# Kernel optimization log

Hardware: AMD Instinct MI355X
Metric: run time of the kernel (lower is better)

Reference implementation:

```python
import jax, jax.numpy as jnp
import numpy as np


def lrelu(x):
    return jax.nn.leaky_relu(x, 0.1)


def mask_softmax(a, mask, axis=-1):
    # faithful to the torch version: max over ALL entries, mask applied post-exp
    a_max = jnp.max(a, axis=axis, keepdims=True)
    e = jnp.exp(a - a_max) * mask
    return e / (jnp.sum(e, axis=axis, keepdims=True) + 1e-6)


def gru_cell(x, h, w_ih, w_hh, b_ih, b_hh):
    # torch.nn.GRUCell math; weights stored as [in, 3H]
    gi = x @ w_ih + b_ih
    gh = h @ w_hh + b_hh
    ir, iz, inn = jnp.split(gi, 3, axis=-1)
    hr, hz, hn = jnp.split(gh, 3, axis=-1)
    r = jax.nn.sigmoid(ir + hr)
    z = jax.nn.sigmoid(iz + hz)
    n = jnp.tanh(inn + r * hn)
    return (1 - z) * n + z * h


def setup_inputs() -> dict:
    key = jax.random.key(0)
    B, N, M, E, H, D, K = 128, 256, 12, 256, 128, 3, 2
    AF, BF, NA, NB = 82, 6, 100, 12
    ks = iter(jax.random.split(key, 64))
    nrm = lambda shape: jax.random.normal(next(ks), shape, jnp.float32) * 0.05
    return dict(
        batch_size=B,
        vertex_mask=jnp.ones((B, N), jnp.float32),
        vertex=jax.random.randint(next(ks), (B, N), 0, NA, dtype=jnp.int32),
        edge=jax.random.randint(next(ks), (B, E), 0, NB, dtype=jnp.int32),
        atom_adj=jax.random.randint(next(ks), (B * N * M,), 0, B * N, dtype=jnp.int32),
        bond_adj=jax.random.randint(next(ks), (B * N * M,), 0, B * E, dtype=jnp.int32),
        nbs_mask=jnp.ones((B, N, M), jnp.float32),
        init_atom_features=nrm((NA, AF)),
        init_bond_features=nrm((NB, BF)),
        emb_w=nrm((AF, H)), emb_b=nrm((H,)),
        Wa_main_w=nrm((D, K, H, H)), Wa_main_b=nrm((D, K, H)),
        Wbmm_w=nrm((D, K, H)), Wbmm_b=nrm((D, K)),
        Wmain_w=nrm((D, K, H, H)), Wmain_b=nrm((D, K, H)),
        Wm2s_w=nrm((D, K * H, H)), Wm2s_b=nrm((D, H)),
        Ws2m_w=nrm((D, H, H)), Ws2m_b=nrm((D, H)),
        Wsuper_w=nrm((D, H, H)), Wsuper_b=nrm((D, H)),
        Wzm1_w=nrm((D, H, H)), Wzm1_b=nrm((D, H)),
        Wzm2_w=nrm((D, H, H)), Wzm2_b=nrm((D, H)),
        Wzs1_w=nrm((D, H, H)), Wzs1_b=nrm((D, H)),
        Wzs2_w=nrm((D, H, H)), Wzs2_b=nrm((D, H)),
        U2_w=nrm((D, H + BF, H)), U2_b=nrm((D, H)),
        U1_w=nrm((D, 2 * H, H)), U1_b=nrm((D, H)),
        gm_wih=nrm((H, 3 * H)), gm_whh=nrm((H, 3 * H)), gm_bih=nrm((3 * H,)), gm_bhh=nrm((3 * H,)),
        gs_wih=nrm((H, 3 * H)), gs_whh=nrm((H, 3 * H)), gs_bih=nrm((3 * H,)), gs_bhh=nrm((3 * H,)),
    )


def reference(batch_size, vertex_mask, vertex, edge, atom_adj, bond_adj, nbs_mask,
              init_atom_features, init_bond_features, emb_w, emb_b,
              Wa_main_w, Wa_main_b, Wbmm_w, Wbmm_b, Wmain_w, Wmain_b,
              Wm2s_w, Wm2s_b, Ws2m_w, Ws2m_b, Wsuper_w, Wsuper_b,
              Wzm1_w, Wzm1_b, Wzm2_w, Wzm2_b, Wzs1_w, Wzs1_b, Wzs2_w, Wzs2_b,
              U2_w, U2_b, U1_w, U1_b,
              gm_wih, gm_whh, gm_bih, gm_bhh, gs_wih, gs_whh, gs_bih, gs_bhh):
    B = batch_size
    N = vertex_mask.shape[1]
    M = nbs_mask.shape[2]
    H = emb_w.shape[1]
    BF = init_bond_features.shape[1]
    D, K = Wa_main_w.shape[0], Wa_main_w.shape[1]

    vertex_initial = init_atom_features[vertex]          # [B,N,AF]
    edge_initial = init_bond_features[edge]              # [B,E,BF]
    vf = lrelu(vertex_initial @ emb_w + emb_b)           # [B,N,H]
    vm = vertex_mask[:, :, None]
    sf = jnp.sum(vf * vm, axis=1, keepdims=True)         # [B,1,H] super node

    for d in range(D):
        # multi-head super-node attention (all k heads vectorized)
        a_main = jnp.tanh(jnp.einsum('bnh,khg->bkng', vf, Wa_main_w[d]) + Wa_main_b[d][None, :, None, :])
        a = jnp.einsum('bkng,kg->bkn', a_main * sf[:, None, :, :], Wbmm_w[d]) + Wbmm_b[d][None, :, None]
        attn = mask_softmax(a, vertex_mask[:, None, :])                  # [B,K,N]
        wv = jnp.einsum('bnh,khg->bkng', vf, Wmain_w[d]) + Wmain_b[d][None, :, None, :]
        m = jnp.einsum('bkn,bkng->bkg', attn, wv).reshape(B, 1, K * H)   # head-concat
        main_to_super = jnp.tanh(m @ Wm2s_w[d] + Wm2s_b[d])              # [B,1,H]

        # WLN unit: gather neighbor atom/bond features, fused MLP + masked sum
        vnei = vf.reshape(-1, H)[atom_adj].reshape(B, N, M, H)
        enei = edge_initial.reshape(-1, BF)[bond_adj].reshape(B, N, M, BF)
        nei = jnp.concatenate([vnei, enei], axis=-1)                     # [B,N,M,H+BF]
        nei_label = lrelu(nei @ U2_w[d] + U2_b[d])
        nei_label = jnp.sum(nei_label * nbs_mask[..., None], axis=-2)    # [B,N,H]
        main_self = lrelu(jnp.concatenate([vf, nei_label], axis=-1) @ U1_w[d] + U1_b[d])

        super_to_main = jnp.tanh(sf @ Ws2m_w[d] + Ws2m_b[d])
        super_self = jnp.tanh(sf @ Wsuper_w[d] + Wsuper_b[d])

        z_main = jax.nn.sigmoid(main_self @ Wzm1_w[d] + Wzm1_b[d]
                                + super_to_main @ Wzm2_w[d] + Wzm2_b[d])
        hidden_main = (1 - z_main) * main_self + z_main * super_to_main
        vf = gru_cell(hidden_main.reshape(-1, H), vf.reshape(-1, H),
                      gm_wih, gm_whh, gm_bih, gm_bhh).reshape(B, N, H)

        z_super = jax.nn.sigmoid(super_self @ Wzs1_w[d] + Wzs1_b[d]
                                 + main_to_super @ Wzs2_w[d] + Wzs2_b[d])
        hidden_super = (1 - z_super) * super_self + z_super * main_to_super
        sf = gru_cell(hidden_super.reshape(B, H), sf.reshape(B, H),
                      gs_wih, gs_whh, gs_bih, gs_bhh).reshape(B, 1, H)

    return (vf, sf)
```

## Files before the change

### kernel.cpp

```cpp
#include <hip/hip_runtime.h>

typedef unsigned short ushort_t;
typedef unsigned int uint_t;
typedef __attribute__((ext_vector_type(8))) short short8;
typedef __attribute__((ext_vector_type(4))) float f32x4;

#define B   128
#define Nv  256
#define Mn  12
#define Hd  128
#define Dd  3
#define Kk  2
#define AFd 82
#define BFd 6
#define BN  (B*Nv)

enum { EPI_NONE = 0, EPI_LRELU = 1 };

__device__ __forceinline__ float lrelu(float x) { return fmaxf(x, 0.1f * x); }
__device__ __forceinline__ float sigmoidf(float x) { return 1.f / (1.f + expf(-x)); }
__device__ __forceinline__ ushort_t f2b(float x) {
    uint_t u = __float_as_uint(x);
    return (ushort_t)((u + 0x7FFFu + ((u >> 16) & 1u)) >> 16);
}
__device__ __forceinline__ float b2f(ushort_t s) {
    return __uint_as_float(((uint_t)s) << 16);
}
__device__ __forceinline__ void b2f4(uint2 u, float* o) {
    o[0] = __uint_as_float((u.x & 0xFFFFu) << 16);
    o[1] = __uint_as_float(u.x & 0xFFFF0000u);
    o[2] = __uint_as_float((u.y & 0xFFFFu) << 16);
    o[3] = __uint_as_float(u.y & 0xFFFF0000u);
}
__device__ __forceinline__ uint_t pk2(float lo, float hi) {
    return (uint_t)f2b(lo) | ((uint_t)f2b(hi) << 16);
}
__device__ __forceinline__ float upk_lo(uint_t u) { return __uint_as_float((u & 0xFFFFu) << 16); }
__device__ __forceinline__ float upk_hi(uint_t u) { return __uint_as_float(u & 0xFFFF0000u); }

struct PrepJob {
    const float* W;
    long sliceStride;
    int K, ldw, nPerSlice, Kspan, KpadRow, kDst, total, outOff, blockStart;
};
struct PrepJobs { PrepJob j[18]; int nJobs; };

__global__ __launch_bounds__(256) void k_prep_all(PrepJobs P, ushort_t* __restrict__ WT)
{
    int bid = blockIdx.x;
    int ji = 0;
    #pragma unroll 1
    while (ji + 1 < P.nJobs && P.j[ji + 1].blockStart <= bid) ++ji;
    const PrepJob J = P.j[ji];
    const int idx = (bid - J.blockStart) * 256 + threadIdx.x;
    if (idx >= J.total) return;
    const int n = idx / J.Kspan, k = idx % J.Kspan;
    const int slice = n / J.nPerSlice, nn = n % J.nPerSlice;
    float v = (k < J.K) ? J.W[(size_t)slice * J.sliceStride + (size_t)k * J.ldw + nn] : 0.f;
    WT[(size_t)J.outOff + (size_t)n * J.KpadRow + J.kDst + k] = f2b(v);
}

__global__ __launch_bounds__(256) void k_qtab(const float* __restrict__ init_bond,
                                              const float* __restrict__ U2w,
                                              ushort_t* __restrict__ qt)
{
    const int d = blockIdx.x;
    const float* W = U2w + (size_t)d * (Hd + BFd) * Hd + (size_t)Hd * Hd;
    ushort_t* q = qt + (size_t)d * 12 * Hd;
    for (int idx = threadIdx.x; idx < 12 * Hd; idx += 256) {
        const int j = idx >> 7, h = idx & 127;
        float s = 0.f;
        #pragma unroll
        for (int f = 0; f < BFd; ++f) s += init_bond[j * BFd + f] * W[f * Hd + h];
        q[idx] = f2b(s);
    }
}

template<int EPI, bool ABF, bool OBF>
__global__ __launch_bounds__(256) void mgemm(
    const void* __restrict__ A1v, int lda1, int K1,
    const int* __restrict__ rowidx,
    const ushort_t* __restrict__ Wt, int Kpad,
    const float* __restrict__ b1,
    void* __restrict__ outv, long ldo)
{
    const int t    = threadIdx.x;
    const int lane = t & 63;
    const int w    = t >> 6;
    const int wm   = w >> 1, wn = w & 1;
    const int lr   = lane & 15, lg = lane >> 4;
    const int row0 = blockIdx.x * 64;

    __shared__ ushort_t As[64 * 64];

    f32x4 acc[2][4];
    #pragma unroll
    for (int i = 0; i < 2; ++i)
        #pragma unroll
        for (int j = 0; j < 4; ++j)
            acc[i][j] = (f32x4){0.f, 0.f, 0.f, 0.f};

    const int r_st = t >> 2, q4 = t & 3;
    const int grow = row0 + r_st;
    const long arow = rowidx ? (long)rowidx[grow] : (long)grow;

    const int nck = Kpad >> 6;
    for (int ck = 0; ck < nck; ++ck) {
        if (ck) __syncthreads();
        {
            const int kb = ck * 64 + q4 * 16;
            union { ushort_t us[16]; uint4 qv[2]; } tmp;
            #pragma unroll
            for (int j = 0; j < 16; ++j) {
                const int kg = kb + j;
                ushort_t v = 0;
                if (kg < K1) {
                    if (ABF) v = ((const ushort_t*)A1v)[(size_t)arow * lda1 + kg];
                    else     v = f2b(((const float*)A1v)[(size_t)arow * lda1 + kg]);
                }
                tmp.us[j] = v;
            }
            #pragma unroll
            for (int j = 0; j < 2; ++j) {
                int byte = r_st * 128 + q4 * 32 + j * 16;
                byte ^= ((r_st & 7) << 4);
                *(uint4*)((char*)As + byte) = tmp.qv[j];
            }
        }
        __syncthreads();
        #pragma unroll
        for (int ks = 0; ks < 64; ks += 32) {
            short8 af[2], bfr[4];
            #pragma unroll
            for (int mf = 0; mf < 2; ++mf) {
                const int row = wm * 32 + mf * 16 + lr;
                int byte = row * 128 + (ks + lg * 8) * 2;
                byte ^= ((row & 7) << 4);
                af[mf] = *(const short8*)((const char*)As + byte);
            }
            #pragma unroll
            for (int nf = 0; nf < 4; ++nf) {
                const int col = wn * 64 + nf * 16 + lr;
                bfr[nf] = *(const short8*)(Wt + (size_t)col * Kpad + ck * 64 + ks + lg * 8);
            }
            #pragma unroll
            for (int mf = 0; mf < 2; ++mf)
                #pragma unroll
                for (int nf = 0; nf < 4; ++nf)
                    acc[mf][nf] = __builtin_amdgcn_mfma_f32_16x16x32_bf16(
                        af[mf], bfr[nf], acc[mf][nf], 0, 0, 0);
        }
    }

    #pragma unroll
    for (int mf = 0; mf < 2; ++mf) {
        #pragma unroll
        for (int nf = 0; nf < 4; ++nf) {
            const int c = wn * 64 + nf * 16 + lr;
            #pragma unroll
            for (int reg = 0; reg < 4; ++reg) {
                const int r = wm * 32 + mf * 16 + lg * 4 + reg;
                const size_t row = (size_t)row0 + r;
                float v = acc[mf][nf][reg];
                if (b1) v += b1[c];
                if constexpr (EPI == EPI_LRELU) v = lrelu(v);
                const size_t oidx = row * ldo + c;
                if (OBF) ((ushort_t*)outv)[oidx] = f2b(v);
                else     ((float*)outv)[oidx] = v;
            }
        }
    }
}

__global__ __launch_bounds__(256) void k_tdp(
    const ushort_t* __restrict__ vfb,
    const ushort_t* __restrict__ Wt,
    const float* __restrict__ waB,
    const float* __restrict__ u2B,
    const float* __restrict__ sf,
    const float* __restrict__ wbmmW,
    const float* __restrict__ wbmmB,
    float* __restrict__ a_out,
    ushort_t* __restrict__ Pout)
{
    const int t = threadIdx.x;
    const int lane = t & 63, w = t >> 6;
    const int wm = w >> 1, wn = w & 1;
    const int lr = lane & 15, lg = lane >> 4;
    const int row0 = blockIdx.x * 64;
    const int ky = blockIdx.y;
    const int b = row0 >> 8;

    __shared__ ushort_t As[64 * 128];
    __shared__ float EUs[128], EBb[128];
    __shared__ float red[64][2];

    {
        const int r_st = t >> 2, q4 = t & 3;
        const ushort_t* src = vfb + (size_t)(row0 + r_st) * Hd + q4 * 32;
        #pragma unroll
        for (int j = 0; j < 4; ++j) {
            uint4 v = ((const uint4*)src)[j];
            int byte = r_st * 256 + q4 * 64 + j * 16;
            byte ^= ((r_st & 7) << 4);
            *(uint4*)((char*)As + byte) = v;
        }
    }
    if (ky != 2 && t < 128) {
        EUs[t] = sf[b * Hd + t] * wbmmW[ky * Hd + t];
        EBb[t] = waB[ky * Hd + t];
    }
    __syncthreads();

    const ushort_t* Wty = Wt + (size_t)ky * 16384;

    f32x4 acc[2][4];
    #pragma unroll
    for (int i = 0; i < 2; ++i)
        #pragma unroll
        for (int j = 0; j < 4; ++j)
            acc[i][j] = (f32x4){0.f, 0.f, 0.f, 0.f};

    #pragma unroll
    for (int kk = 0; kk < 128; kk += 32) {
        short8 af[2], bfr[4];
        #pragma unroll
        for (int nf = 0; nf < 4; ++nf) {
            const int col = wn * 64 + nf * 16 + lr;
            bfr[nf] = *(const short8*)(Wty + (size_t)col * 128 + kk + lg * 8);
        }
        #pragma unroll
        for (int mf = 0; mf < 2; ++mf) {
            const int row = wm * 32 + mf * 16 + lr;
            int byte = row * 256 + (kk + lg * 8) * 2;
            byte ^= ((row & 7) << 4);
            af[mf] = *(const short8*)((const char*)As + byte);
        }
        #pragma unroll
        for (int mf = 0; mf < 2; ++mf)
            #pragma unroll
            for (int nf = 0; nf < 4; ++nf)
                acc[mf][nf] = __builtin_amdgcn_mfma_f32_16x16x32_bf16(
                    af[mf], bfr[nf], acc[mf][nf], 0, 0, 0);
    }

    if (ky == 2) {
        #pragma unroll
        for (int mf = 0; mf < 2; ++mf)
            #pragma unroll
            for (int nf = 0; nf < 4; ++nf) {
                const int c = wn * 64 + nf * 16 + lr;
                #pragma unroll
                for (int reg = 0; reg < 4; ++reg) {
                    const int r = wm * 32 + mf * 16 + lg * 4 + reg;
                    Pout[(size_t)(row0 + r) * Hd + c] = f2b(acc[mf][nf][reg] + u2B[c]);
                }
            }
    } else {
        #pragma unroll
        for (int mf = 0; mf < 2; ++mf) {
            #pragma unroll
            for (int reg = 0; reg < 4; ++reg) {
                float p = 0.f;
                #pragma unroll
                for (int nf = 0; nf < 4; ++nf) {
                    const int c = wn * 64 + nf * 16 + lr;
                    p += tanhf(acc[mf][nf][reg] + EBb[c]) * EUs[c];
                }
                p += __shfl_xor(p, 1); p += __shfl_xor(p, 2);
                p += __shfl_xor(p, 4); p += __shfl_xor(p, 8);
                if (lr == 0) red[wm * 32 + mf * 16 + lg * 4 + reg][wn] = p;
            }
        }
        __syncthreads();
        if (t < 64) {
            const int gr = row0 + t;
            a_out[(size_t)(gr >> 8) * 512 + (size_t)ky * 256 + (gr & 255)] =
                red[t][0] + red[t][1] + wbmmB[ky];
        }
    }
}

__global__ __launch_bounds__(256, 3) void k_mega(
    const ushort_t* __restrict__ vfb,
    const ushort_t* __restrict__ Pb,
    const ushort_t* __restrict__ qt,
    const int* __restrict__ aadj, const int* __restrict__ badj,
    const int* __restrict__ edge, const float* __restrict__ nmask,
    const ushort_t* __restrict__ wt_u1,
    const ushort_t* __restrict__ wt_zm1,
    const ushort_t* __restrict__ wt_rz,
    const ushort_t* __restrict__ wt_inn,
    const ushort_t* __restrict__ wt_hn,
    const float* __restrict__ u1b,
    const float* __restrict__ zm1b,
    const float* __restrict__ bih, const float* __restrict__ bhh,
    const float* __restrict__ czm2, const float* __restrict__ s2m,
    void* __restrict__ outv, const int finalFp32)
{
    const int t = threadIdx.x;
    const int lane = t & 63, w = t >> 6;
    const int wm = w >> 1, wn = w & 1;
    const int lr = lane & 15, lg = lane >> 4;
    const int row0 = blockIdx.x * 64;
    const int b = row0 >> 8;

    __shared__ ushort_t As[64 * 256];
    __shared__ ushort_t aiS[64 * Mn];
    __shared__ ushort_t eiS[64 * Mn];
    __shared__ ushort_t mkS[64 * Mn];

    for (int i = t; i < 64 * Mn; i += 256) {
        const int r = i / Mn, m = i - r * Mn;
        const long g = (long)(row0 + r) * Mn + m;
        aiS[i] = (ushort_t)aadj[g];
        eiS[i] = (ushort_t)edge[badj[g]];
        mkS[i] = f2b(nmask[g]);
    }
    {
        const int r_st = t >> 2, q4 = t & 3;
        const ushort_t* src = vfb + (size_t)(row0 + r_st) * Hd + q4 * 32;
        #pragma unroll
        for (int j = 0; j < 4; ++j) {
            uint4 v = ((const uint4*)src)[j];
            int byte = r_st * 512 + q4 * 64 + j * 16;
            byte ^= ((r_st & 7) << 4);
            *(uint4*)((char*)As + byte) = v;
        }
    }
    __syncthreads();

    #pragma unroll 1
    for (int it = 0; it < 4; ++it) {
        const int idx = it * 256 + t;
        const int r = idx >> 4, h0 = (idx & 15) * 8;
        float a8[8] = {0.f,0.f,0.f,0.f,0.f,0.f,0.f,0.f};
        #pragma unroll
        for (int m = 0; m < Mn; ++m) {
            const int ai = aiS[r * Mn + m];
            const float mk = b2f(mkS[r * Mn + m]);
            const uint4 pv = *(const uint4*)&Pb[(size_t)ai * Hd + h0];
            const uint4 qv = *(const uint4*)&qt[(size_t)eiS[r * Mn + m] * Hd + h0];
            const ushort_t* pp = (const ushort_t*)&pv;
            const ushort_t* qq = (const ushort_t*)&qv;
            #pragma unroll
            for (int e = 0; e < 8; ++e) {
                const float v = b2f(pp[e]) + b2f(qq[e]);
                a8[e] = fmaf(mk, lrelu(v), a8[e]);
            }
        }
        ushort_t o8[8];
        #pragma unroll
        for (int e = 0; e < 8; ++e) o8[e] = f2b(a8[e]);
        int byte = r * 512 + (128 + h0) * 2;
        byte ^= ((r & 7) << 4);
        *(uint4*)((char*)As + byte) = *(const uint4*)o8;
    }
    __syncthreads();

    f32x4 acc[2][4];

#define ZERO_ACC() { _Pragma("unroll") for (int i = 0; i < 2; ++i) _Pragma("unroll") for (int j = 0; j < 4; ++j) acc[i][j] = (f32x4){0.f,0.f,0.f,0.f}; }
#define GEMM_PASS(WG, KPADW, KTOT, AOFF_EXPR) { \
        ZERO_ACC(); \
        _Pragma("unroll") \
        for (int kk = 0; kk < (KTOT); kk += 32) { \
            const int acol = (AOFF_EXPR); \
            short8 af[2], bfr[4]; \
            _Pragma("unroll") \
            for (int nf = 0; nf < 4; ++nf) { \
                const int col = wn * 64 + nf * 16 + lr; \
                bfr[nf] = *(const short8*)((WG) + (size_t)col * (KPADW) + kk + lg * 8); \
            } \
            _Pragma("unroll") \
            for (int mf = 0; mf < 2; ++mf) { \
                const int row = wm * 32 + mf * 16 + lr; \
                int byte = row * 512 + (acol + lg * 8) * 2; \
                byte ^= ((row & 7) << 4); \
                af[mf] = *(const short8*)((const char*)As + byte); \
            } \
            _Pragma("unroll") \
            for (int mf = 0; mf < 2; ++mf) \
                _Pragma("unroll") \
                for (int nf = 0; nf < 4; ++nf) \
                    acc[mf][nf] = __builtin_amdgcn_mfma_f32_16x16x32_bf16(af[mf], bfr[nf], acc[mf][nf], 0, 0, 0); \
        } }

    GEMM_PASS(wt_u1, 256, 256, kk);
    uint_t msp[2][4][2];
    #pragma unroll
    for (int mf = 0; mf < 2; ++mf)
        #pragma unroll
        for (int nf = 0; nf < 4; ++nf) {
            const int c = wn * 64 + nf * 16 + lr;
            const float bb = u1b[c];
            msp[mf][nf][0] = pk2(lrelu(acc[mf][nf][0] + bb), lrelu(acc[mf][nf][1] + bb));
            msp[mf][nf][1] = pk2(lrelu(acc[mf][nf][2] + bb), lrelu(acc[mf][nf][3] + bb));
        }
    __syncthreads();
    #pragma unroll
    for (int mf = 0; mf < 2; ++mf)
        #pragma unroll
        for (int nf = 0; nf < 4; ++nf) {
            const int c = wn * 64 + nf * 16 + lr;
            #pragma unroll
            for (int reg = 0; reg < 4; ++reg) {
                const int row = wm * 32 + mf * 16 + lg * 4 + reg;
                const uint_t pk = msp[mf][nf][reg >> 1];
                const ushort_t msb = (reg & 1) ? (ushort_t)(pk >> 16) : (ushort_t)(pk & 0xFFFFu);
                int byte = row * 512 + (128 + c) * 2;
                byte ^= ((row & 7) << 4);
                *(ushort_t*)((char*)As + byte) = msb;
            }
        }
    __syncthreads();

    GEMM_PASS(wt_zm1, 128, 128, 128 + kk);
    uint_t zpk[2][4][2];
    #pragma unroll
    for (int mf = 0; mf < 2; ++mf)
        #pragma unroll
        for (int nf = 0; nf < 4; ++nf) {
            const int c = wn * 64 + nf * 16 + lr;
            const float bb = zm1b[c] + czm2[b * Hd + c];
            zpk[mf][nf][0] = pk2(sigmoidf(acc[mf][nf][0] + bb), sigmoidf(acc[mf][nf][1] + bb));
            zpk[mf][nf][1] = pk2(sigmoidf(acc[mf][nf][2] + bb), sigmoidf(acc[mf][nf][3] + bb));
        }
    __syncthreads();
    #pragma unroll
    for (int mf = 0; mf < 2; ++mf)
        #pragma unroll
        for (int nf = 0; nf < 4; ++nf) {
            const int c = wn * 64 + nf * 16 + lr;
            const float s2 = s2m[b * Hd + c];
            #pragma unroll
            for (int reg = 0; reg < 4; ++reg) {
                const int row = wm * 32 + mf * 16 + lg * 4 + reg;
                const uint_t mpk = msp[mf][nf][reg >> 1];
                const uint_t zp  = zpk[mf][nf][reg >> 1];
                const float ms = (reg & 1) ? upk_hi(mpk) : upk_lo(mpk);
                const float z  = (reg & 1) ? upk_hi(zp)  : upk_lo(zp);
                const float hid = (1.f - z) * ms + z * s2;
                int byte = row * 512 + (128 + c) * 2;
                byte ^= ((row & 7) << 4);
                *(ushort_t*)((char*)As + byte) = f2b(hid);
            }
        }
    __syncthreads();

    uint_t innp[2][4][2], hnp[2][4][2];
    GEMM_PASS(wt_inn, 128, 128, 128 + kk);
    #pragma unroll
    for (int mf = 0; mf < 2; ++mf)
        #pragma unroll
        for (int nf = 0; nf < 4; ++nf) {
            const int c = wn * 64 + nf * 16 + lr;
            const float bb = bih[256 + c];
            innp[mf][nf][0] = pk2(acc[mf][nf][0] + bb, acc[mf][nf][1] + bb);
            innp[mf][nf][1] = pk2(acc[mf][nf][2] + bb, acc[mf][nf][3] + bb);
        }
    GEMM_PASS(wt_hn, 128, 128, kk);
    #pragma unroll
    for (int mf = 0; mf < 2; ++mf)
        #pragma unroll
        for (int nf = 0; nf < 4; ++nf) {
            const int c = wn * 64 + nf * 16 + lr;
            const float bb = bhh[256 + c];
            hnp[mf][nf][0] = pk2(acc[mf][nf][0] + bb, acc[mf][nf][1] + bb);
            hnp[mf][nf][1] = pk2(acc[mf][nf][2] + bb, acc[mf][nf][3] + bb);
        }
    GEMM_PASS(wt_rz, 256, 256, (kk < 128) ? (128 + kk) : (kk - 128));
    #pragma unroll
    for (int mf = 0; mf < 2; ++mf)
        #pragma unroll
        for (int nf = 0; nf < 4; ++nf) {
            const int c = wn * 64 + nf * 16 + lr;
            const float bb = bih[c] + bhh[c];
            const float r0 = sigmoidf(acc[mf][nf][0] + bb);
            const float r1 = sigmoidf(acc[mf][nf][1] + bb);
            const float r2 = sigmoidf(acc[mf][nf][2] + bb);
            const float r3 = sigmoidf(acc[mf][nf][3] + bb);
            const float n0 = tanhf(upk_lo(innp[mf][nf][0]) + r0 * upk_lo(hnp[mf][nf][0]));
            const float n1 = tanhf(upk_hi(innp[mf][nf][0]) + r1 * upk_hi(hnp[mf][nf][0]));
            const float n2 = tanhf(upk_lo(innp[mf][nf][1]) + r2 * upk_lo(hnp[mf][nf][1]));
            const float n3 = tanhf(upk_hi(innp[mf][nf][1]) + r3 * upk_hi(hnp[mf][nf][1]));
            innp[mf][nf][0] = pk2(n0, n1);
            innp[mf][nf][1] = pk2(n2, n3);
        }
    GEMM_PASS(wt_rz + 128 * 256, 256, 256, (kk < 128) ? (128 + kk) : (kk - 128));
    #pragma unroll
    for (int mf = 0; mf < 2; ++mf)
        #pragma unroll
        for (int nf = 0; nf < 4; ++nf) {
            const int c = wn * 64 + nf * 16 + lr;
            const float bb = bih[128 + c] + bhh[128 + c];
            #pragma unroll
            for (int reg = 0; reg < 4; ++reg) {
                const int rl = wm * 32 + mf * 16 + lg * 4 + reg;
                const float z = sigmoidf(acc[mf][nf][reg] + bb);
                const uint_t np = innp[mf][nf][reg >> 1];
                const float n = (reg & 1) ? upk_hi(np) : upk_lo(np);
                int byte = rl * 512 + c * 2;
                byte ^= ((rl & 7) << 4);
                const float h = b2f(*(const ushort_t*)((const char*)As + byte));
                const float o = (1.f - z) * n + z * h;
                const size_t oidx = (size_t)(row0 + rl) * Hd + c;
                if (finalFp32) ((float*)outv)[oidx] = o;
                else           ((ushort_t*)outv)[oidx] = f2b(o);
            }
        }
#undef GEMM_PASS
#undef ZERO_ACC
}

__device__ __forceinline__ void gemv128(const float* __restrict__ W, int ldw, int off,
                                        const float* __restrict__ x, int K,
                                        float (*red)[32][4], float* __restrict__ y, int t)
{
    const int gq = t & 31, hs = t >> 5;
    const int hn = K >> 3;
    f32x4 acc = (f32x4){0.f, 0.f, 0.f, 0.f};
    const float* Wp = W + (size_t)off + (size_t)gq * 4;
    const int h0 = hs * hn;
    #pragma unroll 8
    for (int i = 0; i < hn; ++i) {
        const float4 wv = *(const float4*)&Wp[(size_t)(h0 + i) * ldw];
        const float xv = x[h0 + i];
        acc.x = fmaf(xv, wv.x, acc.x);
        acc.y = fmaf(xv, wv.y, acc.y);
        acc.z = fmaf(xv, wv.z, acc.z);
        acc.w = fmaf(xv, wv.w, acc.w);
    }
    *(f32x4*)&red[hs][gq][0] = acc;
    __syncthreads();
    if (t < 128) {
        float s = 0.f;
        #pragma unroll
        for (int p = 0; p < 8; ++p) s += red[p][t >> 2][t & 3];
        y[t] = s;
    }
    __syncthreads();
}

__global__ __launch_bounds__(256) void k_super(
    const float* __restrict__ a_buf, const float* __restrict__ vmask,
    const ushort_t* __restrict__ vfb,
    const float* __restrict__ sf_in,
    const float* __restrict__ Wm, const float* __restrict__ bm,
    const float* __restrict__ Wm2s, const float* __restrict__ bm2s,
    const float* __restrict__ Ws2m, const float* __restrict__ bs2m,
    const float* __restrict__ Wsup, const float* __restrict__ bsup,
    const float* __restrict__ Wzm2, const float* __restrict__ bzm2,
    const float* __restrict__ Wzs1, const float* __restrict__ bzs1,
    const float* __restrict__ Wzs2, const float* __restrict__ bzs2,
    const float* __restrict__ gwih, const float* __restrict__ gwhh,
    const float* __restrict__ gbih, const float* __restrict__ gbhh,
    float* __restrict__ s2m_g, float* __restrict__ czm2_g,
    float* __restrict__ sf_out)
{
    const int b = blockIdx.x, t = threadIdx.x;
    const int wid = t >> 6, lane = t & 63;
    __shared__ float red[8][32][4];
    __shared__ float att0[256], att1[256];
    __shared__ float sfl[128], tbA[128], tbB[128], mv[256];
    __shared__ float ms2[128], s2ml[128], ssl[128], hsl[128], tmp1[128], tmp2[128];
    __shared__ float gib[384], ghb[384];
    __shared__ float saS[2];
    __shared__ float lm[4][2], ls[4][2];

    const float v0 = a_buf[(size_t)b * 512 + t];
    const float v1 = a_buf[(size_t)b * 512 + 256 + t];
    const float vm = vmask[b * Nv + t];
    float m0 = v0, m1 = v1;
    #pragma unroll
    for (int o = 1; o < 64; o <<= 1) {
        m0 = fmaxf(m0, __shfl_xor(m0, o));
        m1 = fmaxf(m1, __shfl_xor(m1, o));
    }
    if (lane == 0) { lm[wid][0] = m0; lm[wid][1] = m1; }
    __syncthreads();
    m0 = fmaxf(fmaxf(lm[0][0], lm[1][0]), fmaxf(lm[2][0], lm[3][0]));
    m1 = fmaxf(fmaxf(lm[0][1], lm[1][1]), fmaxf(lm[2][1], lm[3][1]));
    const float e0v = expf(v0 - m0) * vm;
    const float e1v = expf(v1 - m1) * vm;
    float s0 = e0v, s1 = e1v;
    #pragma unroll
    for (int o = 1; o < 64; o <<= 1) {
        s0 += __shfl_xor(s0, o);
        s1 += __shfl_xor(s1, o);
    }
    if (lane == 0) { ls[wid][0] = s0; ls[wid][1] = s1; }
    if (t < 128) sfl[t] = sf_in[b * Hd + t];
    __syncthreads();
    s0 = ls[0][0] + ls[1][0] + ls[2][0] + ls[3][0];
    s1 = ls[0][1] + ls[1][1] + ls[2][1] + ls[3][1];
    att0[t] = e0v / (s0 + 1e-6f);
    att1[t] = e1v / (s1 + 1e-6f);
    if (t == 0) { saS[0] = s0 / (s0 + 1e-6f); saS[1] = s1 / (s1 + 1e-6f); }
    __syncthreads();

    {
        const int hq = t & 31, ns = t >> 5;
        f32x4 a0 = (f32x4){0.f,0.f,0.f,0.f}, a1 = (f32x4){0.f,0.f,0.f,0.f};
        const ushort_t* base = vfb + (size_t)b * Nv * Hd + hq * 4;
        #pragma unroll 8
        for (int i = 0; i < 32; ++i) {
            const int n = ns * 32 + i;
            float xv[4];
            b2f4(*(const uint2*)&base[(size_t)n * Hd], xv);
            const float w0 = att0[n], w1 = att1[n];
            a0.x = fmaf(w0, xv[0], a0.x); a0.y = fmaf(w0, xv[1], a0.y);
            a0.z = fmaf(w0, xv[2], a0.z); a0.w = fmaf(w0, xv[3], a0.w);
            a1.x = fmaf(w1, xv[0], a1.x); a1.y = fmaf(w1, xv[1], a1.y);
            a1.z = fmaf(w1, xv[2], a1.z); a1.w = fmaf(w1, xv[3], a1.w);
        }
        *(f32x4*)&red[ns][hq][0] = a0;
        __syncthreads();
        if (t < 128) { float s = 0.f;
            #pragma unroll
            for (int p = 0; p < 8; ++p) s += red[p][t >> 2][t & 3];
            tbA[t] = s; }
        __syncthreads();
        *(f32x4*)&red[ns][hq][0] = a1;
        __syncthreads();
        if (t < 128) { float s = 0.f;
            #pragma unroll
            for (int p = 0; p < 8; ++p) s += red[p][t >> 2][t & 3];
            tbB[t] = s; }
        __syncthreads();
    }

    gemv128(Wm, Hd, 0, tbA, Hd, red, mv, t);
    gemv128(Wm + Hd * Hd, Hd, 0, tbB, Hd, red, mv + 128, t);
    mv[t] += saS[t >> 7] * bm[t];
    __syncthreads();

    gemv128(Wm2s, Hd, 0, mv, 2 * Hd, red, tmp1, t);
    if (t < 128) ms2[t] = tanhf(tmp1[t] + bm2s[t]);
    __syncthreads();

    gemv128(Ws2m, Hd, 0, sfl, Hd, red, tmp1, t);
    if (t < 128) { const float v = tanhf(tmp1[t] + bs2m[t]); s2ml[t] = v; s2m_g[b * Hd + t] = v; }
    __syncthreads();
    gemv128(Wsup, Hd, 0, sfl, Hd, red, tmp1, t);
    if (t < 128) ssl[t] = tanhf(tmp1[t] + bsup[t]);
    __syncthreads();

    gemv128(Wzm2, Hd, 0, s2ml, Hd, red, tmp1, t);
    if (t < 128) czm2_g[b * Hd + t] = tmp1[t] + bzm2[t];

    gemv128(Wzs1, Hd, 0, ssl, Hd, red, tmp1, t);
    gemv128(Wzs2, Hd, 0, ms2, Hd, red, tmp2, t);
    if (t < 128) {
        const float zs = sigmoidf(tmp1[t] + bzs1[t] + tmp2[t] + bzs2[t]);
        hsl[t] = (1.f - zs) * ssl[t] + zs * ms2[t];
    }
    __syncthreads();

    #pragma unroll 1
    for (int c = 0; c < 3; ++c) {
        gemv128(gwih, 3 * Hd, c * Hd, hsl, Hd, red, tmp1, t);
        if (t < 128) gib[c * Hd + t] = tmp1[t] + gbih[c * Hd + t];
        gemv128(gwhh, 3 * Hd, c * Hd, sfl, Hd, red, tmp2, t);
        if (t < 128) ghb[c * Hd + t] = tmp2[t] + gbhh[c * Hd + t];
    }
    __syncthreads();
    if (t < 128) {
        const float r = sigmoidf(gib[t] + ghb[t]);
        const float z = sigmoidf(gib[128 + t] + ghb[128 + t]);
        const float n = tanhf(gib[256 + t] + r * ghb[256 + t]);
        sf_out[b * Hd + t] = (1.f - z) * n + z * sfl[t];
    }
}

__global__ __launch_bounds__(256) void k_sfv(const ushort_t* __restrict__ vfb,
                                             const float* __restrict__ vmask,
                                             float* __restrict__ sf)
{
    const int b = blockIdx.x, t = threadIdx.x;
    __shared__ float vm[256];
    __shared__ float red[8][32][4];
    vm[t] = vmask[b * Nv + t];
    __syncthreads();
    const int hq = t & 31, ns = t >> 5;
    f32x4 acc = (f32x4){0.f,0.f,0.f,0.f};
    const ushort_t* base = vfb + (size_t)b * Nv * Hd + hq * 4;
    #pragma unroll 8
    for (int i = 0; i < 32; ++i) {
        const int n = ns * 32 + i;
        float xv[4];
        b2f4(*(const uint2*)&base[(size_t)n * Hd], xv);
        const float w = vm[n];
        acc.x = fmaf(w, xv[0], acc.x); acc.y = fmaf(w, xv[1], acc.y);
        acc.z = fmaf(w, xv[2], acc.z); acc.w = fmaf(w, xv[3], acc.w);
    }
    *(f32x4*)&red[ns][hq][0] = acc;
    __syncthreads();
    if (t < 128) {
        float s = 0.f;
        #pragma unroll
        for (int p = 0; p < 8; ++p) s += red[p][t >> 2][t & 3];
        sf[b * Hd + t] = s;
    }
}

__global__ __launch_bounds__(256) void k_copy(const float* __restrict__ src,
                                              float* __restrict__ dst, int n)
{
    const int i = blockIdx.x * 256 + threadIdx.x;
    if (i < n) dst[i] = src[i];
}

extern "C" void kernel_launch(void* const* d_in, const int* in_sizes, int n_in,
                              void* d_out, int out_size, void* d_ws, size_t ws_size,
                              hipStream_t stream)
{
    (void)in_sizes; (void)n_in; (void)out_size;

    const float* vertex_mask = (const float*)d_in[1];
    const int*   vertex      = (const int*)d_in[2];
    const int*   edge        = (const int*)d_in[3];
    const int*   atom_adj    = (const int*)d_in[4];
    const int*   bond_adj    = (const int*)d_in[5];
    const float* nbs_mask    = (const float*)d_in[6];
    const float* init_atom   = (const float*)d_in[7];
    const float* init_bond   = (const float*)d_in[8];
    const float* emb_w  = (const float*)d_in[9];
    const float* emb_b  = (const float*)d_in[10];
    const float* Wa_w   = (const float*)d_in[11];
    const float* Wa_b   = (const float*)d_in[12];
    const float* Wbmm_w = (const float*)d_in[13];
    const float* Wbmm_b = (const float*)d_in[14];
    const float* Wm_w   = (const float*)d_in[15];
    const float* Wm_b   = (const float*)d_in[16];
    const float* Wm2s_w = (const float*)d_in[17];
    const float* Wm2s_b = (const float*)d_in[18];
    const float* Ws2m_w = (const float*)d_in[19];
    const float* Ws2m_b = (const float*)d_in[20];
    const float* Wsup_w = (const float*)d_in[21];
    const float* Wsup_b = (const float*)d_in[22];
    const float* Wzm1_w = (const float*)d_in[23];
    const float* Wzm1_b = (const float*)d_in[24];
    const float* Wzm2_w = (const float*)d_in[25];
    const float* Wzm2_b = (const float*)d_in[26];
    const float* Wzs1_w = (const float*)d_in[27];
    const float* Wzs1_b = (const float*)d_in[28];
    const float* Wzs2_w = (const float*)d_in[29];
    const float* Wzs2_b = (const float*)d_in[30];
    const float* U2_w   = (const float*)d_in[31];
    const float* U2_b   = (const float*)d_in[32];
    const float* U1_w   = (const float*)d_in[33];
    const float* U1_b   = (const float*)d_in[34];
    const float* gm_wih = (const float*)d_in[35];
    const float* gm_whh = (const float*)d_in[36];
    const float* gm_bih = (const float*)d_in[37];
    const float* gm_bhh = (const float*)d_in[38];
    const float* gs_wih = (const float*)d_in[39];
    const float* gs_whh = (const float*)d_in[40];
    const float* gs_bih = (const float*)d_in[41];
    const float* gs_bhh = (const float*)d_in[42];

    const size_t MB = 1u << 20;
    if (ws_size < 40 * MB) return;

    char* base = (char*)d_ws;
    ushort_t* VF0 = (ushort_t*)base;
    ushort_t* VF1 = (ushort_t*)(base + 8 * MB);
    ushort_t* Pb  = (ushort_t*)(base + 16 * MB);
    ushort_t* WT  = (ushort_t*)(base + 24 * MB);
    ushort_t* QT  = (ushort_t*)(base + 26 * MB);
    float*    S   = (float*)(base + 27 * MB);

    float* sfA    = S;
    float* sfB    = S + 16384;
    float* a_buf  = S + 32768;
    float* s2m    = S + 98304;
    float* c_zm2  = S + 114688;

    float* X1 = (float*)d_out;
    float* sf_final = X1 + (size_t)BN * Hd;

    const int OFF_EMB = 0;
    const int PERD = 98304;
    const int OFF_L0 = 16384;
    const int OFF_RZ = OFF_L0 + 3 * PERD;
    const int OFF_NH = OFF_RZ + 65536;

    PrepJobs PJ;
    int nj = 0, blk0 = 0;
    auto addJob = [&](const float* W, int K, int ldw, long sStride, int nPer,
                      int Kspan, int KpadRow, int kDst, int ncols, int outOff) {
        PrepJob& J = PJ.j[nj++];
        J.W = W; J.K = K; J.ldw = ldw; J.sliceStride = sStride; J.nPerSlice = nPer;
        J.Kspan = Kspan; J.KpadRow = KpadRow; J.kDst = kDst;
        J.total = ncols * Kspan; J.outOff = outOff; J.blockStart = blk0;
        blk0 += (J.total + 255) / 256;
    };
    addJob(emb_w, AFd, Hd, 0, Hd, 128, 128, 0, 128, OFF_EMB);
    for (int d = 0; d < Dd; ++d) {
        const int o = OFF_L0 + d * PERD;
        addJob(Wa_w + (long)d * Kk * Hd * Hd, Hd, Hd, (long)Hd * Hd, Hd, 128, 128, 0, 256, o);
        addJob(U2_w + (long)d * (Hd + BFd) * Hd, Hd, Hd, 0, Hd, 128, 128, 0, 128, o + 32768);
        addJob(U1_w + (long)d * 2 * Hd * Hd, 2 * Hd, Hd, 0, Hd, 256, 256, 0, 128, o + 49152);
        addJob(Wzm1_w + (long)d * Hd * Hd, Hd, Hd, 0, Hd, 128, 128, 0, 128, o + 81920);
    }
    addJob(gm_wih, Hd, 3 * Hd, 0, 256, 128, 256, 0,   256, OFF_RZ);
    addJob(gm_whh, Hd, 3 * Hd, 0, 256, 128, 256, 128, 256, OFF_RZ);
    addJob(gm_wih + 256, Hd, 3 * Hd, 0, 128, 128, 128, 0, 128, OFF_NH);
    addJob(gm_whh + 256, Hd, 3 * Hd, 0, 128, 128, 128, 0, 128, OFF_NH + 16384);
    PJ.nJobs = nj;
    k_prep_all<<<dim3(blk0), dim3(256), 0, stream>>>(PJ, WT);
    k_qtab<<<dim3(Dd), dim3(256), 0, stream>>>(init_bond, U2_w, QT);

    const dim3 blk(256);
    const dim3 g1(BN / 64, 1);

    mgemm<EPI_LRELU, false, true><<<g1, blk, 0, stream>>>(
        init_atom, AFd, AFd, vertex,
        WT + OFF_EMB, 128, emb_b, VF0, Hd);
    k_sfv<<<dim3(B), blk, 0, stream>>>(VF0, vertex_mask, sfA);

    for (int d = 0; d < Dd; ++d) {
        ushort_t* vin  = (d & 1) ? VF1 : VF0;
        ushort_t* vout = (d & 1) ? VF0 : VF1;
        float* sin  = (d & 1) ? sfB : sfA;
        float* sout = (d & 1) ? sfA : sfB;

        const int o = OFF_L0 + d * PERD;

        k_tdp<<<dim3(BN / 64, 3), blk, 0, stream>>>(
            vin, WT + o,
            Wa_b + (long)d * Kk * Hd, U2_b + (long)d * Hd,
            sin, Wbmm_w + (long)d * Kk * Hd, Wbmm_b + (long)d * Kk,
            a_buf, Pb);

        k_super<<<dim3(B), blk, 0, stream>>>(
            a_buf, vertex_mask, vin, sin,
            Wm_w + (long)d * Kk * Hd * Hd, Wm_b + (long)d * Kk * Hd,
            Wm2s_w + (long)d * Kk * Hd * Hd, Wm2s_b + (long)d * Hd,
            Ws2m_w + (long)d * Hd * Hd, Ws2m_b + (long)d * Hd,
            Wsup_w + (long)d * Hd * Hd, Wsup_b + (long)d * Hd,
            Wzm2_w + (long)d * Hd * Hd, Wzm2_b + (long)d * Hd,
            Wzs1_w + (long)d * Hd * Hd, Wzs1_b + (long)d * Hd,
            Wzs2_w + (long)d * Hd * Hd, Wzs2_b + (long)d * Hd,
            gs_wih, gs_whh, gs_bih, gs_bhh,
            s2m, c_zm2, sout);

        k_mega<<<g1, blk, 0, stream>>>(
            vin, Pb, QT + (size_t)d * 12 * Hd,
            atom_adj, bond_adj, edge, nbs_mask,
            WT + o + 49152, WT + o + 81920,
            WT + OFF_RZ, WT + OFF_NH, WT + OFF_NH + 16384,
            U1_b + (long)d * Hd, Wzm1_b + (long)d * Hd,
            gm_bih, gm_bhh,
            c_zm2, s2m,
            (d == Dd - 1) ? (void*)X1 : (void*)vout, (d == Dd - 1) ? 1 : 0);
    }

    k_copy<<<dim3((B * Hd + 255) / 256), blk, 0, stream>>>(sfB, sf_final, B * Hd);
}
```

Measured before the change: 350.7 us.

## Shrink k_mega tile to 32 rows and read vertex features from global

```diff
diff --git a/kernel.cpp b/kernel.cpp
--- a/kernel.cpp
+++ b/kernel.cpp
@@ -191,26 +191,13 @@
     const int ky = blockIdx.y;
     const int b = row0 >> 8;
 
-    __shared__ ushort_t As[64 * 128];
     __shared__ float EUs[128], EBb[128];
     __shared__ float red[64][2];
 
-    {
-        const int r_st = t >> 2, q4 = t & 3;
-        const ushort_t* src = vfb + (size_t)(row0 + r_st) * Hd + q4 * 32;
-        #pragma unroll
-        for (int j = 0; j < 4; ++j) {
-            uint4 v = ((const uint4*)src)[j];
-            int byte = r_st * 256 + q4 * 64 + j * 16;
-            byte ^= ((r_st & 7) << 4);
-            *(uint4*)((char*)As + byte) = v;
-        }
-    }
     if (ky != 2 && t < 128) {
         EUs[t] = sf[b * Hd + t] * wbmmW[ky * Hd + t];
         EBb[t] = waB[ky * Hd + t];
     }
-    __syncthreads();
 
     const ushort_t* Wty = Wt + (size_t)ky * 16384;
 
@@ -230,12 +217,8 @@
             bfr[nf] = *(const short8*)(Wty + (size_t)col * 128 + kk + lg * 8);
         }
         #pragma unroll
-        for (int mf = 0; mf < 2; ++mf) {
-            const int row = wm * 32 + mf * 16 + lr;
-            int byte = row * 256 + (kk + lg * 8) * 2;
-            byte ^= ((row & 7) << 4);
-            af[mf] = *(const short8*)((const char*)As + byte);
-        }
+        for (int mf = 0; mf < 2; ++mf)
+            af[mf] = *(const short8*)(vfb + (size_t)(row0 + wm * 32 + mf * 16 + lr) * Hd + kk + lg * 8);
         #pragma unroll
         for (int mf = 0; mf < 2; ++mf)
             #pragma unroll
@@ -257,6 +240,7 @@
                 }
             }
     } else {
+        __syncthreads();
         #pragma unroll
         for (int mf = 0; mf < 2; ++mf) {
             #pragma unroll
@@ -281,7 +265,7 @@
     }
 }
 
-__global__ __launch_bounds__(256, 3) void k_mega(
+__global__ __launch_bounds__(256, 4) void k_mega(
     const ushort_t* __restrict__ vfb,
     const ushort_t* __restrict__ Pb,
     const ushort_t* __restrict__ qt,
@@ -299,39 +283,28 @@
     void* __restrict__ outv, const int finalFp32)
 {
     const int t = threadIdx.x;
-    const int lane = t & 63, w = t >> 6;
-    const int wm = w >> 1, wn = w & 1;
+    const int lane = t & 63;
+    const int wn = t >> 6;
     const int lr = lane & 15, lg = lane >> 4;
-    const int row0 = blockIdx.x * 64;
+    const int row0 = blockIdx.x * 32;
     const int b = row0 >> 8;
 
-    __shared__ ushort_t As[64 * 256];
-    __shared__ ushort_t aiS[64 * Mn];
-    __shared__ ushort_t eiS[64 * Mn];
-    __shared__ ushort_t mkS[64 * Mn];
-
-    for (int i = t; i < 64 * Mn; i += 256) {
+    __shared__ ushort_t As[32 * 256];
+    __shared__ ushort_t aiS[32 * Mn];
+    __shared__ ushort_t eiS[32 * Mn];
+    __shared__ ushort_t mkS[32 * Mn];
+
+    for (int i = t; i < 32 * Mn; i += 256) {
         const int r = i / Mn, m = i - r * Mn;
         const long g = (long)(row0 + r) * Mn + m;
         aiS[i] = (ushort_t)aadj[g];
         eiS[i] = (ushort_t)edge[badj[g]];
         mkS[i] = f2b(nmask[g]);
     }
-    {
-        const int r_st = t >> 2, q4 = t & 3;
-        const ushort_t* src = vfb + (size_t)(row0 + r_st) * Hd + q4 * 32;
-        #pragma unroll
-        for (int j = 0; j < 4; ++j) {
-            uint4 v = ((const uint4*)src)[j];
-            int byte = r_st * 512 + q4 * 64 + j * 16;
-            byte ^= ((r_st & 7) << 4);
-            *(uint4*)((char*)As + byte) = v;
-        }
-    }
     __syncthreads();
 
     #pragma unroll 1
-    for (int it = 0; it < 4; ++it) {
+    for (int it = 0; it < 2; ++it) {
         const int idx = it * 256 + t;
         const int r = idx >> 4, h0 = (idx & 15) * 8;
         float a8[8] = {0.f,0.f,0.f,0.f,0.f,0.f,0.f,0.f};
@@ -352,60 +325,54 @@
         ushort_t o8[8];
         #pragma unroll
         for (int e = 0; e < 8; ++e) o8[e] = f2b(a8[e]);
-        int byte = r * 512 + (128 + h0) * 2;
+        int byte = r * 512 + h0 * 2;
         byte ^= ((r & 7) << 4);
         *(uint4*)((char*)As + byte) = *(const uint4*)o8;
     }
     __syncthreads();
 
-    f32x4 acc[2][4];
-
-#define ZERO_ACC() { _Pragma("unroll") for (int i = 0; i < 2; ++i) _Pragma("unroll") for (int j = 0; j < 4; ++j) acc[i][j] = (f32x4){0.f,0.f,0.f,0.f}; }
-#define GEMM_PASS(WG, KPADW, KTOT, AOFF_EXPR) { \
+    f32x4 acc[2][2];
+
+#define AF_G(KC) (*(const short8*)(vfb + (size_t)(row0 + mf * 16 + lr) * Hd + (KC) + lg * 8))
+#define AF_L(LC) (*(const short8*)((const char*)As + ((((mf * 16 + lr) * 512 + ((LC) + lg * 8) * 2)) ^ ((lr & 7) << 4))))
+#define ZERO_ACC() { _Pragma("unroll") for (int i = 0; i < 2; ++i) _Pragma("unroll") for (int j = 0; j < 2; ++j) acc[i][j] = (f32x4){0.f,0.f,0.f,0.f}; }
+#define GEMM_PASS(WG, KPADW, KTOT, A_EXPR) { \
         ZERO_ACC(); \
         _Pragma("unroll") \
         for (int kk = 0; kk < (KTOT); kk += 32) { \
-            const int acol = (AOFF_EXPR); \
-            short8 af[2], bfr[4]; \
+            short8 af[2], bfv[2]; \
             _Pragma("unroll") \
-            for (int nf = 0; nf < 4; ++nf) { \
-                const int col = wn * 64 + nf * 16 + lr; \
-                bfr[nf] = *(const short8*)((WG) + (size_t)col * (KPADW) + kk + lg * 8); \
-            } \
+            for (int nf = 0; nf < 2; ++nf) \
+                bfv[nf] = *(const short8*)((WG) + (size_t)(wn * 32 + nf * 16 + lr) * (KPADW) + kk + lg * 8); \
             _Pragma("unroll") \
-            for (int mf = 0; mf < 2; ++mf) { \
-                const int row = wm * 32 + mf * 16 + lr; \
-                int byte = row * 512 + (acol + lg * 8) * 2; \
-                byte ^= ((row & 7) << 4); \
-                af[mf] = *(const short8*)((const char*)As + byte); \
-            } \
+            for (int mf = 0; mf < 2; ++mf) \
+                af[mf] = (A_EXPR); \
             _Pragma("unroll") \
             for (int mf = 0; mf < 2; ++mf) \
                 _Pragma("unroll") \
-                for (int nf = 0; nf < 4; ++nf) \
-                    acc[mf][nf] = __builtin_amdgcn_mfma_f32_16x16x32_bf16(af[mf], bfr[nf], acc[mf][nf], 0, 0, 0); \
+                for (int nf = 0; nf < 2; ++nf) \
+                    acc[mf][nf] = __builtin_amdgcn_mfma_f32_16x16x32_bf16(af[mf], bfv[nf], acc[mf][nf], 0, 0, 0); \
         } }
 
-    GEMM_PASS(wt_u1, 256, 256, kk);
-    uint_t msp[2][4][2];
+    GEMM_PASS(wt_u1, 256, 256, (kk < 128) ? AF_G(kk) : AF_L(kk - 128));
+    uint_t msp[2][2][2];
     #pragma unroll
     for (int mf = 0; mf < 2; ++mf)
         #pragma unroll
-        for (int nf = 0; nf < 4; ++nf) {
-            const int c = wn * 64 + nf * 16 + lr;
+        for (int nf = 0; nf < 2; ++nf) {
+            const int c = wn * 32 + nf * 16 + lr;
             const float bb = u1b[c];
             msp[mf][nf][0] = pk2(lrelu(acc[mf][nf][0] + bb), lrelu(acc[mf][nf][1] + bb));
             msp[mf][nf][1] = pk2(lrelu(acc[mf][nf][2] + bb), lrelu(acc[mf][nf][3] + bb));
         }
-    __syncthreads();
     #pragma unroll
     for (int mf = 0; mf < 2; ++mf)
         #pragma unroll
-        for (int nf = 0; nf < 4; ++nf) {
-            const int c = wn * 64 + nf * 16 + lr;
+        for (int nf = 0; nf < 2; ++nf) {
+            const int c = wn * 32 + nf * 16 + lr;
             #pragma unroll
             for (int reg = 0; reg < 4; ++reg) {
-                const int row = wm * 32 + mf * 16 + lg * 4 + reg;
+                const int row = mf * 16 + lg * 4 + reg;
                 const uint_t pk = msp[mf][nf][reg >> 1];
                 const ushort_t msb = (reg & 1) ? (ushort_t)(pk >> 16) : (ushort_t)(pk & 0xFFFFu);
                 int byte = row * 512 + (128 + c) * 2;
@@ -415,66 +382,55 @@
         }
     __syncthreads();
 
-    GEMM_PASS(wt_zm1, 128, 128, 128 + kk);
-    uint_t zpk[2][4][2];
+    GEMM_PASS(wt_zm1, 128, 128, AF_L(128 + kk));
     #pragma unroll
     for (int mf = 0; mf < 2; ++mf)
         #pragma unroll
-        for (int nf = 0; nf < 4; ++nf) {
-            const int c = wn * 64 + nf * 16 + lr;
+        for (int nf = 0; nf < 2; ++nf) {
+            const int c = wn * 32 + nf * 16 + lr;
             const float bb = zm1b[c] + czm2[b * Hd + c];
-            zpk[mf][nf][0] = pk2(sigmoidf(acc[mf][nf][0] + bb), sigmoidf(acc[mf][nf][1] + bb));
-            zpk[mf][nf][1] = pk2(sigmoidf(acc[mf][nf][2] + bb), sigmoidf(acc[mf][nf][3] + bb));
-        }
-    __syncthreads();
-    #pragma unroll
-    for (int mf = 0; mf < 2; ++mf)
-        #pragma unroll
-        for (int nf = 0; nf < 4; ++nf) {
-            const int c = wn * 64 + nf * 16 + lr;
             const float s2 = s2m[b * Hd + c];
             #pragma unroll
             for (int reg = 0; reg < 4; ++reg) {
-                const int row = wm * 32 + mf * 16 + lg * 4 + reg;
+                const int row = mf * 16 + lg * 4 + reg;
+                const float z = sigmoidf(acc[mf][nf][reg] + bb);
                 const uint_t mpk = msp[mf][nf][reg >> 1];
-                const uint_t zp  = zpk[mf][nf][reg >> 1];
                 const float ms = (reg & 1) ? upk_hi(mpk) : upk_lo(mpk);
-                const float z  = (reg & 1) ? upk_hi(zp)  : upk_lo(zp);
                 const float hid = (1.f - z) * ms + z * s2;
-                int byte = row * 512 + (128 + c) * 2;
+                int byte = row * 512 + c * 2;
                 byte ^= ((row & 7) << 4);
                 *(ushort_t*)((char*)As + byte) = f2b(hid);
             }
         }
     __syncthreads();
 
-    uint_t innp[2][4][2], hnp[2][4][2];
-    GEMM_PASS(wt_inn, 128, 128, 128 + kk);
+    uint_t innp[2][2][2], hnp[2][2][2];
+    GEMM_PASS(wt_inn, 128, 128, AF_L(kk));
     #pragma unroll
     for (int mf = 0; mf < 2; ++mf)
         #pragma unroll
-        for (int nf = 0; nf < 4; ++nf) {
-            const int c = wn * 64 + nf * 16 + lr;
+        for (int nf = 0; nf < 2; ++nf) {
+            const int c = wn * 32 + nf * 16 + lr;
             const float bb = bih[256 + c];
             innp[mf][nf][0] = pk2(acc[mf][nf][0] + bb, acc[mf][nf][1] + bb);
             innp[mf][nf][1] = pk2(acc[mf][nf][2] + bb, acc[mf][nf][3] + bb);
         }
-    GEMM_PASS(wt_hn, 128, 128, kk);
+    GEMM_PASS(wt_hn, 128, 128, AF_G(kk));
     #pragma unroll
     for (int mf = 0; mf < 2; ++mf)
         #pragma unroll
-        for (int nf = 0; nf < 4; ++nf) {
-            const int c = wn * 64 + nf * 16 + lr;
+        for (int nf = 0; nf < 2; ++nf) {
+            const int c = wn * 32 + nf * 16 + lr;
             const float bb = bhh[256 + c];
             hnp[mf][nf][0] = pk2(acc[mf][nf][0] + bb, acc[mf][nf][1] + bb);
             hnp[mf][nf][1] = pk2(acc[mf][nf][2] + bb, acc[mf][nf][3] + bb);
         }
-    GEMM_PASS(wt_rz, 256, 256, (kk < 128) ? (128 + kk) : (kk - 128));
+    GEMM_PASS(wt_rz, 256, 256, (kk < 128) ? AF_L(kk) : AF_G(kk - 128));
     #pragma unroll
     for (int mf = 0; mf < 2; ++mf)
         #pragma unroll
-        for (int nf = 0; nf < 4; ++nf) {
-            const int c = wn * 64 + nf * 16 + lr;
+        for (int nf = 0; nf < 2; ++nf) {
+            const int c = wn * 32 + nf * 16 + lr;
             const float bb = bih[c] + bhh[c];
             const float r0 = sigmoidf(acc[mf][nf][0] + bb);
             const float r1 = sigmoidf(acc[mf][nf][1] + bb);
@@ -487,22 +443,20 @@
             innp[mf][nf][0] = pk2(n0, n1);
             innp[mf][nf][1] = pk2(n2, n3);
         }
-    GEMM_PASS(wt_rz + 128 * 256, 256, 256, (kk < 128) ? (128 + kk) : (kk - 128));
+    GEMM_PASS(wt_rz + 128 * 256, 256, 256, (kk < 128) ? AF_L(kk) : AF_G(kk - 128));
     #pragma unroll
     for (int mf = 0; mf < 2; ++mf)
         #pragma unroll
-        for (int nf = 0; nf < 4; ++nf) {
-            const int c = wn * 64 + nf * 16 + lr;
+        for (int nf = 0; nf < 2; ++nf) {
+            const int c = wn * 32 + nf * 16 + lr;
             const float bb = bih[128 + c] + bhh[128 + c];
             #pragma unroll
             for (int reg = 0; reg < 4; ++reg) {
-                const int rl = wm * 32 + mf * 16 + lg * 4 + reg;
+                const int rl = mf * 16 + lg * 4 + reg;
                 const float z = sigmoidf(acc[mf][nf][reg] + bb);
                 const uint_t np = innp[mf][nf][reg >> 1];
                 const float n = (reg & 1) ? upk_hi(np) : upk_lo(np);
-                int byte = rl * 512 + c * 2;
-                byte ^= ((rl & 7) << 4);
-                const float h = b2f(*(const ushort_t*)((const char*)As + byte));
+                const float h = b2f(vfb[(size_t)(row0 + rl) * Hd + c]);
                 const float o = (1.f - z) * n + z * h;
                 const size_t oidx = (size_t)(row0 + rl) * Hd + c;
                 if (finalFp32) ((float*)outv)[oidx] = o;
@@ -511,6 +465,8 @@
         }
 #undef GEMM_PASS
 #undef ZERO_ACC
+#undef AF_G
+#undef AF_L
 }
 
 __device__ __forceinline__ void gemv128(const float* __restrict__ W, int ldw, int off,
@@ -813,9 +769,8 @@
     k_qtab<<<dim3(Dd), dim3(256), 0, stream>>>(init_bond, U2_w, QT);
 
     const dim3 blk(256);
-    const dim3 g1(BN / 64, 1);
-
-    mgemm<EPI_LRELU, false, true><<<g1, blk, 0, stream>>>(
+
+    mgemm<EPI_LRELU, false, true><<<dim3(BN / 64), blk, 0, stream>>>(
         init_atom, AFd, AFd, vertex,
         WT + OFF_EMB, 128, emb_b, VF0, Hd);
     k_sfv<<<dim3(B), blk, 0, stream>>>(VF0, vertex_mask, sfA);
@@ -846,7 +801,7 @@
             gs_wih, gs_whh, gs_bih, gs_bhh,
             s2m, c_zm2, sout);
 
-        k_mega<<<g1, blk, 0, stream>>>(
+        k_mega<<<dim3(BN / 32), blk, 0, stream>>>(
             vin, Pb, QT + (size_t)d * 12 * Hd,
             atom_adj, bond_adj, edge, nbs_mask,
             WT + o + 49152, WT + o + 81920,
```

Measured after the change: 379.5 us. 8.2% more time.
